# Optimization experiments

Measured on AMD Instinct MI355X. Metric: run time of the kernel, lower is better.

The kernel has to match this reference:

```python
import jax, jax.numpy as jnp
import numpy as np
from jax import lax

H = 100  # hidden size (hardcoded in the module)


def _lstm_cell(x, h, c, W_ih, W_hh, b):
    # gates: [B, 4H] in PyTorch order i, f, g, o
    gates = x @ W_ih.T + h @ W_hh.T + b
    i, f, g, o = jnp.split(gates, 4, axis=-1)
    c = jax.nn.sigmoid(f) * c + jax.nn.sigmoid(i) * jnp.tanh(g)
    h = jax.nn.sigmoid(o) * jnp.tanh(c)
    return h, c


def setup_inputs() -> dict:
    key = jax.random.key(0)
    ks = jax.random.split(key, 12)
    B, T = 512, 1000
    s = 0.1  # keep gates away from saturation
    return {
        "input": jax.random.normal(ks[0], (B, T), dtype=jnp.float32),
        "W_ih1": jax.random.normal(ks[1], (4 * H, 1), dtype=jnp.float32) * s,
        "W_hh1": jax.random.normal(ks[2], (4 * H, H), dtype=jnp.float32) * s,
        "b_ih1": jax.random.normal(ks[3], (4 * H,), dtype=jnp.float32) * s,
        "b_hh1": jax.random.normal(ks[4], (4 * H,), dtype=jnp.float32) * s,
        "W_ih2": jax.random.normal(ks[5], (4 * H, H), dtype=jnp.float32) * s,
        "W_hh2": jax.random.normal(ks[6], (4 * H, H), dtype=jnp.float32) * s,
        "b_ih2": jax.random.normal(ks[7], (4 * H,), dtype=jnp.float32) * s,
        "b_hh2": jax.random.normal(ks[8], (4 * H,), dtype=jnp.float32) * s,
        "W_lin": jax.random.normal(ks[9], (1, H), dtype=jnp.float32) * s,
        "b_lin": jax.random.normal(ks[10], (1,), dtype=jnp.float32) * s,
        "future": 300,
    }


def reference(input, W_ih1, W_hh1, b_ih1, b_hh1, W_ih2, W_hh2, b_ih2, b_hh2,
              W_lin, b_lin, future):
    B = input.shape[0]
    b1 = b_ih1 + b_hh1
    b2 = b_ih2 + b_hh2
    xs = input.T[:, :, None]  # [T, B, 1]
    z = jnp.zeros((B, H), dtype=input.dtype)

    def step(carry, x):
        h1, c1, h2, c2 = carry
        h1, c1 = _lstm_cell(x, h1, c1, W_ih1, W_hh1, b1)
        h2, c2 = _lstm_cell(h1, h2, c2, W_ih2, W_hh2, b2)
        y = h2 @ W_lin.T + b_lin  # [B, 1]
        return (h1, c1, h2, c2), y

    carry, ys = lax.scan(step, (z, z, z, z), xs)  # ys: [T, B, 1]

    def fstep(carry, _):
        h1, c1, h2, c2, y = carry
        h1, c1 = _lstm_cell(y, h1, c1, W_ih1, W_hh1, b1)
        h2, c2 = _lstm_cell(h1, h2, c2, W_ih2, W_hh2, b2)
        y = h2 @ W_lin.T + b_lin
        return (h1, c1, h2, c2, y), y

    h1, c1, h2, c2 = carry
    _, ys_f = lax.scan(fstep, (h1, c1, h2, c2, ys[-1]), None, length=future)

    out = jnp.concatenate([ys, ys_f], axis=0)  # [T+future, B, 1]
    return out[:, :, 0].T  # [B, T+future]
```

## Files before the change

kernel.cpp:

```cpp
#include <hip/hip_runtime.h>
#include <stdint.h>

#define HID 100
#define B_TOTAL 512
#define T_IN 1000
#define NB 2
#define BLOCK 512

typedef __fp16 f16x8 __attribute__((ext_vector_type(8)));
typedef float f32x4 __attribute__((ext_vector_type(4)));

#define MF(A, B, C) __builtin_amdgcn_mfma_f32_16x16x32_f16((A), (B), (C), 0, 0, 0)
#define Z4 ((f32x4){0.f, 0.f, 0.f, 0.f})

#if __has_builtin(__builtin_amdgcn_exp2f)
#define EXP2F(x) __builtin_amdgcn_exp2f(x)
#else
#define EXP2F(x) exp2f(x)
#endif
#if __has_builtin(__builtin_amdgcn_rcpf)
#define RCPF(x) __builtin_amdgcn_rcpf(x)
#else
#define RCPF(x) (1.0f / (x))
#endif
#define LOG2E 1.44269504f
__device__ __forceinline__ float sigm(float x) { return RCPF(1.0f + EXP2F(-LOG2E * x)); }
__device__ __forceinline__ float tanh_fast(float x) {
  return 1.0f - 2.0f * RCPF(EXP2F((2.0f * LOG2E) * x) + 1.0f);
}

__device__ __forceinline__ int jmap(int tl, int m) { return (m & 3) * 100 + 4 * tl + (m >> 2); }

__device__ __forceinline__ __fp16 w1e(const float* Whh1, const float* Wih1,
                                      const float* bih1, const float* bhh1, int j, int k) {
  if (k < 100) return (__fp16)Whh1[j * 100 + k];
  if (k == 100) return (__fp16)Wih1[j];
  if (k == 101 || k == 102) {
    float b = bih1[j] + bhh1[j];
    __fp16 hi = (__fp16)b;
    return (k == 101) ? hi : (__fp16)(b - (float)hi);
  }
  return (__fp16)0.0f;
}
__device__ __forceinline__ __fp16 w2e(const float* Wih2, const float* Whh2,
                                      const float* bih2, const float* bhh2, int j, int k) {
  if (k < 100) return (__fp16)Wih2[j * 100 + k];
  if (k == 101 || k == 102) {
    float b = bih2[j] + bhh2[j];
    __fp16 hi = (__fp16)b;
    return (k == 101) ? hi : (__fp16)(b - (float)hi);
  }
  if (k >= 112 && k < 212) return (__fp16)Whh2[j * 100 + (k - 112)];
  return (__fp16)0.0f;
}

__device__ __forceinline__ f16x8 mka1(const float* Whh1, const float* Wih1,
                                      const float* bih1, const float* bhh1,
                                      int tl, int kt, int m, int kg) {
  int j = jmap(tl, m);
  f16x8 r;
#pragma unroll
  for (int e = 0; e < 8; e++) r[e] = w1e(Whh1, Wih1, bih1, bhh1, j, kt * 32 + kg * 8 + e);
  return r;
}
__device__ __forceinline__ f16x8 mka2(const float* Wih2, const float* Whh2,
                                      const float* bih2, const float* bhh2,
                                      int tl, int kt, int m, int kg) {
  int j = jmap(tl, m);
  f16x8 r;
#pragma unroll
  for (int e = 0; e < 8; e++) r[e] = w2e(Wih2, Whh2, bih2, bhh2, j, kt * 32 + kg * 8 + e);
  return r;
}

__global__ __launch_bounds__(BLOCK, 2) void lstm2_mfma(
    const float* __restrict__ input,
    const float* __restrict__ Wih1,
    const float* __restrict__ Whh1,
    const float* __restrict__ bih1,
    const float* __restrict__ bhh1,
    const float* __restrict__ Wih2,
    const float* __restrict__ Whh2,
    const float* __restrict__ bih2,
    const float* __restrict__ bhh2,
    const float* __restrict__ Wlin,
    const float* __restrict__ blin,
    const int* __restrict__ futp,
    float* __restrict__ out)
{
  __shared__ __align__(16) __fp16 H1X[2][NB][128];
  __shared__ __align__(16) __fp16 H2s[2][NB][112];
  __shared__ __align__(16) float  ybuf[2][NB][104];
  __shared__ __align__(16) float  xrow[NB][T_IN];
  __shared__ __align__(16) __fp16 T24[11 * 64 * 8];
  __shared__ float wls[104];

  const int tid = threadIdx.x;
  const int lane = tid & 63;
  const int wv = tid >> 6;
  const int b0 = blockIdx.x * NB;
  const int F = futp[0];
  const int TT = T_IN + F;

  for (int i = tid; i < NB * T_IN; i += BLOCK) {
    int b = i / T_IN, tt = i % T_IN;
    xrow[b][tt] = input[(size_t)(b0 + b) * T_IN + tt];
  }
  { uint32_t* z = (uint32_t*)H1X; if (tid < 256) z[tid] = 0u; }
  { uint32_t* z = (uint32_t*)H2s; if (tid < 224) z[tid] = 0u; }
  { float* z = (float*)ybuf; if (tid < 416) z[tid] = 0.0f; }
  if (tid < 104) wls[tid] = (tid < HID) ? Wlin[tid] : 0.0f;

  const int n15 = lane & 15;
  const int kg = lane >> 4;
  const int bcol = lane & 1;

  const int sel = lane & 15;
  const int cg  = sel >> 1;
  const int ab  = sel & 1;
  const int aq  = lane >> 4;
  const int atl = (cg == 0) ? wv : (cg == 1) ? 8 + wv : (cg == 2) ? 16 + wv : 24;
  const int ak  = atl * 4 + aq;
  const bool awr1 = (sel < 6) || (wv == 0 && sel < 8);
  const bool awr2 = (sel < 6) || (wv == 1 && sel < 8);
  float c1v = 0.0f, c2v = 0.0f;

  const int is_y = (tid >= 496);
  const int ybat = ((tid - 496) >> 3) & 1;
  const int yl = (tid - 496) & 7;
  const float blin0 = blin[0];

  f16x8 W1f0[4], W1f1[4], W1f2[4], W2f0[7], W2f1[7], W2f2[7];
#pragma unroll
  for (int kt = 0; kt < 4; kt++) {
    W1f0[kt] = mka1(Whh1, Wih1, bih1, bhh1, wv, kt, n15, kg);
    W1f1[kt] = mka1(Whh1, Wih1, bih1, bhh1, 8 + wv, kt, n15, kg);
    W1f2[kt] = mka1(Whh1, Wih1, bih1, bhh1, 16 + wv, kt, n15, kg);
  }
#pragma unroll
  for (int kt = 0; kt < 7; kt++) {
    W2f0[kt] = mka2(Wih2, Whh2, bih2, bhh2, wv, kt, n15, kg);
    W2f1[kt] = mka2(Wih2, Whh2, bih2, bhh2, 8 + wv, kt, n15, kg);
    W2f2[kt] = mka2(Wih2, Whh2, bih2, bhh2, 16 + wv, kt, n15, kg);
  }
  if (tid < 64) {
    f16x8* TV = (f16x8*)T24;
    const int m_ = tid & 15, kg_ = tid >> 4;
#pragma unroll
    for (int kt = 0; kt < 4; kt++) TV[kt * 64 + tid] = mka1(Whh1, Wih1, bih1, bhh1, 24, kt, m_, kg_);
#pragma unroll
    for (int kt = 0; kt < 3; kt++) TV[(4 + kt) * 64 + tid] = mka2(Wih2, Whh2, bih2, bhh2, 24, 4 + kt, m_, kg_);
#pragma unroll
    for (int kt = 0; kt < 4; kt++) TV[(7 + kt) * 64 + tid] = mka2(Wih2, Whh2, bih2, bhh2, 24, kt, m_, kg_);
  }

  __syncthreads();
  if (tid < 4) { H1X[tid >> 1][tid & 1][101] = (__fp16)1.0f; H1X[tid >> 1][tid & 1][102] = (__fp16)1.0f; }
  if (tid >= 4 && tid < 6) H1X[1][tid - 4][100] = (__fp16)xrow[tid - 4][0];
  __syncthreads();

  f16x8 bL1[4], bH2[3], bL2[4];
  f32x4 c0, c1, c2, c3, d0, d1, d2, d3;

#define RD_L1(P) { _Pragma("unroll") for (int kt_ = 0; kt_ < 4; kt_++) \
    bL1[kt_] = *(const f16x8*)&H1X[P][bcol][kt_ * 32 + kg * 8]; }
#define RD_H2P(P) { _Pragma("unroll") for (int kt_ = 0; kt_ < 3; kt_++) \
    bH2[kt_] = *(const f16x8*)&H2s[P][bcol][16 + kt_ * 32 + kg * 8]; }
#define RD_L2(PH1, PH2) { _Pragma("unroll") for (int kt_ = 0; kt_ < 4; kt_++) { \
    const int k0_ = kt_ * 32 + kg * 8; \
    const __fp16* sp_ = (k0_ < 112) ? &H1X[PH1][bcol][k0_] : &H2s[PH2][bcol][k0_ - 112]; \
    bL2[kt_] = *(const f16x8*)sp_; } }

#define MFMA_L1 { \
    c0 = Z4; c1 = Z4; c2 = Z4; c3 = Z4; \
    _Pragma("unroll") for (int kt_ = 0; kt_ < 4; kt_++) { \
      c0 = MF(W1f0[kt_], bL1[kt_], c0); c1 = MF(W1f1[kt_], bL1[kt_], c1); c2 = MF(W1f2[kt_], bL1[kt_], c2); } \
    if (wv == 0) { const f16x8* TV = (const f16x8*)T24; \
      _Pragma("unroll") for (int kt_ = 0; kt_ < 4; kt_++) c3 = MF(TV[kt_ * 64 + lane], bL1[kt_], c3); } }

#define MFMA_L2 { \
    d0 = Z4; d1 = Z4; d2 = Z4; d3 = Z4; \
    _Pragma("unroll") for (int kt_ = 0; kt_ < 4; kt_++) { \
      d0 = MF(W2f0[kt_], bL2[kt_], d0); d1 = MF(W2f1[kt_], bL2[kt_], d1); d2 = MF(W2f2[kt_], bL2[kt_], d2); } \
    _Pragma("unroll") for (int kt_ = 0; kt_ < 3; kt_++) { \
      d0 = MF(W2f0[kt_ + 4], bH2[kt_], d0); d1 = MF(W2f1[kt_ + 4], bH2[kt_], d1); d2 = MF(W2f2[kt_ + 4], bH2[kt_], d2); } \
    if (wv == 1) { const f16x8* TV = (const f16x8*)T24; \
      _Pragma("unroll") for (int kt_ = 0; kt_ < 4; kt_++) d3 = MF(TV[(7 + kt_) * 64 + lane], bL2[kt_], d3); \
      _Pragma("unroll") for (int kt_ = 0; kt_ < 3; kt_++) d3 = MF(TV[(4 + kt_) * 64 + lane], bH2[kt_], d3); } }

#define ACT1(W_) { \
    f32x4 qq = (cg == 0) ? c0 : (cg == 1) ? c1 : (cg == 2) ? c2 : c3; \
    float sf_ = sigm(qq[1]), si_ = sigm(qq[0]), tg_ = tanh_fast(qq[2]); \
    c1v = sf_ * c1v + si_ * tg_; \
    float h_ = sigm(qq[3]) * tanh_fast(c1v); \
    if (awr1) H1X[W_][ab][ak] = (__fp16)h_; }

#define ACT2(W_) { \
    f32x4 qq = (cg == 0) ? d0 : (cg == 1) ? d1 : (cg == 2) ? d2 : d3; \
    float sf_ = sigm(qq[1]), si_ = sigm(qq[0]), tg_ = tanh_fast(qq[2]); \
    c2v = sf_ * c2v + si_ * tg_; \
    float h_ = sigm(qq[3]) * tanh_fast(c2v); \
    if (awr2) { H2s[W_][ab][ak] = (__fp16)h_; ybuf[W_][ab][ak] = h_; } }

#define Y_BODY(tt, RP, FEED, FP) { \
    const float* yb_ = &ybuf[RP][ybat][0]; \
    float s = 0.0f; \
    _Pragma("unroll") \
    for (int m = 0; m < 13; m++) s = fmaf(yb_[yl + 8 * m], wls[yl + 8 * m], s); \
    s += __shfl_down(s, 4, 8); \
    s += __shfl_down(s, 2, 8); \
    s += __shfl_down(s, 1, 8); \
    if (yl == 0) { \
      float y = s + blin0; \
      out[(size_t)(b0 + ybat) * TT + (tt)] = y; \
      if (FEED) H1X[FP][ybat][100] = (__fp16)y; } }

  RD_L1(1)
  MFMA_L1
  ACT1(0)
  if (tid >= 80 && tid < 82) H1X[0][tid - 80][100] = (__fp16)xrow[tid - 80][1];
  __syncthreads();

  for (int t = 0; t < T_IN - 1; t++) {
    const int p = t & 1, w = p ^ 1;
    RD_L1(p) RD_L2(p, p) RD_H2P(p)
    MFMA_L2
    MFMA_L1
    if (is_y && t > 0) Y_BODY(t - 1, p, 0, 0)
    if (tid >= 80 && tid < 82 && t + 2 < T_IN)
      H1X[w][tid - 80][100] = (__fp16)xrow[tid - 80][t + 2];
    ACT2(w)
    ACT1(w)
    __syncthreads();
  }

  for (int t = T_IN - 1; t < TT; t++) {
    const int P = t & 1, W = P ^ 1;
    RD_L2(P, P) RD_H2P(P)
    MFMA_L2
    if (is_y && t == T_IN - 1) Y_BODY(t - 1, P, 0, 0)
    ACT2(W)
    __syncthreads();
    if (is_y) Y_BODY(t, W, (t + 1) < TT, P)
    if (t + 1 >= TT) break;
    __syncthreads();
    RD_L1(P)
    MFMA_L1
    ACT1(W)
    __syncthreads();
  }
}

extern "C" void kernel_launch(void* const* d_in, const int* in_sizes, int n_in,
                              void* d_out, int out_size, void* d_ws, size_t ws_size,
                              hipStream_t stream) {
  const float* input = (const float*)d_in[0];
  const float* Wih1  = (const float*)d_in[1];
  const float* Whh1  = (const float*)d_in[2];
  const float* bih1  = (const float*)d_in[3];
  const float* bhh1  = (const float*)d_in[4];
  const float* Wih2  = (const float*)d_in[5];
  const float* Whh2  = (const float*)d_in[6];
  const float* bih2  = (const float*)d_in[7];
  const float* bhh2  = (const float*)d_in[8];
  const float* Wlin  = (const float*)d_in[9];
  const float* blin  = (const float*)d_in[10];
  const int*   futp  = (const int*)d_in[11];
  float* out = (float*)d_out;

  dim3 grid(B_TOTAL / NB);
  dim3 block(BLOCK);
  hipLaunchKernelGGL(lstm2_mfma, grid, block, 0, stream,
                     input, Wih1, Whh1, bih1, bhh1, Wih2, Whh2, bih2, bhh2,
                     Wlin, blin, futp, out);
}
```

Baseline: 1.660 ms.

## Restructure autoregressive phase to overlap layer-1 MFMA and compute output redundantly per wave

In the future-prediction loop, the layer-1 recurrent MFMA now runs alongside the layer-2 MFMA, with the x input column zeroed out of the weights. Each wave computes the linear output y itself with fdot2 over H2 from shared memory plus cross-lane shuffles, then adds y·W_ih1 as a rank-1 fma in the activation. This removes one barrier and the serial Y_BODY→L1 dependency per future step. Layer-2 operand reads also reuse the layer-1 h fragments instead of reloading them, and the shared buffers get a wider row stride.

```diff
diff --git a/kernel.cpp b/kernel.cpp
--- a/kernel.cpp
+++ b/kernel.cpp
@@ -6,8 +6,10 @@
 #define T_IN 1000
 #define NB 2
 #define BLOCK 512
+#define RSTR 160
 
 typedef __fp16 f16x8 __attribute__((ext_vector_type(8)));
+typedef __fp16 f16x2 __attribute__((ext_vector_type(2)));
 typedef float f32x4 __attribute__((ext_vector_type(4)));
 
 #define MF(A, B, C) __builtin_amdgcn_mfma_f32_16x16x32_f16((A), (B), (C), 0, 0, 0)
@@ -27,6 +29,21 @@
 __device__ __forceinline__ float sigm(float x) { return RCPF(1.0f + EXP2F(-LOG2E * x)); }
 __device__ __forceinline__ float tanh_fast(float x) {
   return 1.0f - 2.0f * RCPF(EXP2F((2.0f * LOG2E) * x) + 1.0f);
+}
+
+__device__ __forceinline__ float dot8(f16x8 a, f16x8 b, float acc) {
+#if __has_builtin(__builtin_amdgcn_fdot2)
+#pragma unroll
+  for (int q = 0; q < 4; q++) {
+    f16x2 xa = {a[2 * q], a[2 * q + 1]};
+    f16x2 xb = {b[2 * q], b[2 * q + 1]};
+    acc = __builtin_amdgcn_fdot2(xa, xb, acc, false);
+  }
+#else
+#pragma unroll
+  for (int e = 0; e < 8; e++) acc = fmaf((float)a[e], (float)b[e], acc);
+#endif
+  return acc;
 }
 
 __device__ __forceinline__ int jmap(int tl, int m) { return (m & 3) * 100 + 4 * tl + (m >> 2); }
@@ -88,8 +105,8 @@
     const int* __restrict__ futp,
     float* __restrict__ out)
 {
-  __shared__ __align__(16) __fp16 H1X[2][NB][128];
-  __shared__ __align__(16) __fp16 H2s[2][NB][112];
+  __shared__ __align__(16) __fp16 H1X[2][NB][RSTR];
+  __shared__ __align__(16) __fp16 H2s[2][NB][RSTR];
   __shared__ __align__(16) float  ybuf[2][NB][104];
   __shared__ __align__(16) float  xrow[NB][T_IN];
   __shared__ __align__(16) __fp16 T24[11 * 64 * 8];
@@ -106,8 +123,8 @@
     int b = i / T_IN, tt = i % T_IN;
     xrow[b][tt] = input[(size_t)(b0 + b) * T_IN + tt];
   }
-  { uint32_t* z = (uint32_t*)H1X; if (tid < 256) z[tid] = 0u; }
-  { uint32_t* z = (uint32_t*)H2s; if (tid < 224) z[tid] = 0u; }
+  { uint32_t* z = (uint32_t*)H1X; if (tid < 320) z[tid] = 0u; }
+  { uint32_t* z = (uint32_t*)H2s; if (tid < 320) z[tid] = 0u; }
   { float* z = (float*)ybuf; if (tid < 416) z[tid] = 0.0f; }
   if (tid < 104) wls[tid] = (tid < HID) ? Wlin[tid] : 0.0f;
 
@@ -130,6 +147,19 @@
   const int yl = (tid - 496) & 7;
   const float blin0 = blin[0];
 
+  f16x8 wlinv[4];
+#pragma unroll
+  for (int i = 0; i < 4; i++) {
+#pragma unroll
+    for (int e = 0; e < 8; e++) {
+      int k = i * 32 + kg * 8 + e;
+      wlinv[i][e] = (__fp16)((k < HID) ? Wlin[k] : 0.f);
+    }
+  }
+  f32x4 wih1q;
+#pragma unroll
+  for (int g = 0; g < 4; g++) wih1q[g] = Wih1[g * 100 + ak];
+
   f16x8 W1f0[4], W1f1[4], W1f2[4], W2f0[7], W2f1[7], W2f2[7];
 #pragma unroll
   for (int kt = 0; kt < 4; kt++) {
@@ -159,50 +189,59 @@
   if (tid >= 4 && tid < 6) H1X[1][tid - 4][100] = (__fp16)xrow[tid - 4][0];
   __syncthreads();
 
-  f16x8 bL1[4], bH2[3], bL2[4];
+  f16x8 bH1a[4], bH2[3], bl2m;
   f32x4 c0, c1, c2, c3, d0, d1, d2, d3;
 
-#define RD_L1(P) { _Pragma("unroll") for (int kt_ = 0; kt_ < 4; kt_++) \
-    bL1[kt_] = *(const f16x8*)&H1X[P][bcol][kt_ * 32 + kg * 8]; }
+#define RD_H1A(P) { _Pragma("unroll") for (int kt_ = 0; kt_ < 4; kt_++) \
+    bH1a[kt_] = *(const f16x8*)&H1X[P][bcol][kt_ * 32 + kg * 8]; }
+#define RD_L2M(P) { f16x8 hm_ = *(const f16x8*)&H2s[P][bcol][(kg >= 2) ? ((kg - 2) * 8) : 0]; \
+    bl2m = (kg >= 2) ? hm_ : bH1a[3]; }
 #define RD_H2P(P) { _Pragma("unroll") for (int kt_ = 0; kt_ < 3; kt_++) \
     bH2[kt_] = *(const f16x8*)&H2s[P][bcol][16 + kt_ * 32 + kg * 8]; }
-#define RD_L2(PH1, PH2) { _Pragma("unroll") for (int kt_ = 0; kt_ < 4; kt_++) { \
-    const int k0_ = kt_ * 32 + kg * 8; \
-    const __fp16* sp_ = (k0_ < 112) ? &H1X[PH1][bcol][k0_] : &H2s[PH2][bcol][k0_ - 112]; \
-    bL2[kt_] = *(const f16x8*)sp_; } }
 
 #define MFMA_L1 { \
     c0 = Z4; c1 = Z4; c2 = Z4; c3 = Z4; \
     _Pragma("unroll") for (int kt_ = 0; kt_ < 4; kt_++) { \
-      c0 = MF(W1f0[kt_], bL1[kt_], c0); c1 = MF(W1f1[kt_], bL1[kt_], c1); c2 = MF(W1f2[kt_], bL1[kt_], c2); } \
+      c0 = MF(W1f0[kt_], bH1a[kt_], c0); c1 = MF(W1f1[kt_], bH1a[kt_], c1); c2 = MF(W1f2[kt_], bH1a[kt_], c2); } \
     if (wv == 0) { const f16x8* TV = (const f16x8*)T24; \
-      _Pragma("unroll") for (int kt_ = 0; kt_ < 4; kt_++) c3 = MF(TV[kt_ * 64 + lane], bL1[kt_], c3); } }
+      _Pragma("unroll") for (int kt_ = 0; kt_ < 4; kt_++) c3 = MF(TV[kt_ * 64 + lane], bH1a[kt_], c3); } }
 
 #define MFMA_L2 { \
     d0 = Z4; d1 = Z4; d2 = Z4; d3 = Z4; \
-    _Pragma("unroll") for (int kt_ = 0; kt_ < 4; kt_++) { \
-      d0 = MF(W2f0[kt_], bL2[kt_], d0); d1 = MF(W2f1[kt_], bL2[kt_], d1); d2 = MF(W2f2[kt_], bL2[kt_], d2); } \
+    _Pragma("unroll") for (int kt_ = 0; kt_ < 3; kt_++) { \
+      d0 = MF(W2f0[kt_], bH1a[kt_], d0); d1 = MF(W2f1[kt_], bH1a[kt_], d1); d2 = MF(W2f2[kt_], bH1a[kt_], d2); } \
+    d0 = MF(W2f0[3], bl2m, d0); d1 = MF(W2f1[3], bl2m, d1); d2 = MF(W2f2[3], bl2m, d2); \
     _Pragma("unroll") for (int kt_ = 0; kt_ < 3; kt_++) { \
       d0 = MF(W2f0[kt_ + 4], bH2[kt_], d0); d1 = MF(W2f1[kt_ + 4], bH2[kt_], d1); d2 = MF(W2f2[kt_ + 4], bH2[kt_], d2); } \
     if (wv == 1) { const f16x8* TV = (const f16x8*)T24; \
-      _Pragma("unroll") for (int kt_ = 0; kt_ < 4; kt_++) d3 = MF(TV[(7 + kt_) * 64 + lane], bL2[kt_], d3); \
+      _Pragma("unroll") for (int kt_ = 0; kt_ < 3; kt_++) d3 = MF(TV[(7 + kt_) * 64 + lane], bH1a[kt_], d3); \
+      d3 = MF(TV[10 * 64 + lane], bl2m, d3); \
       _Pragma("unroll") for (int kt_ = 0; kt_ < 3; kt_++) d3 = MF(TV[(4 + kt_) * 64 + lane], bH2[kt_], d3); } }
 
-#define ACT1(W_) { \
+#define ACT1_TF(W_) { \
     f32x4 qq = (cg == 0) ? c0 : (cg == 1) ? c1 : (cg == 2) ? c2 : c3; \
     float sf_ = sigm(qq[1]), si_ = sigm(qq[0]), tg_ = tanh_fast(qq[2]); \
     c1v = sf_ * c1v + si_ * tg_; \
     float h_ = sigm(qq[3]) * tanh_fast(c1v); \
     if (awr1) H1X[W_][ab][ak] = (__fp16)h_; }
 
-#define ACT2(W_) { \
+#define ACT1_AR(W_, YV_) { \
+    f32x4 qq = (cg == 0) ? c0 : (cg == 1) ? c1 : (cg == 2) ? c2 : c3; \
+    qq[0] = fmaf(wih1q[0], (YV_), qq[0]); qq[1] = fmaf(wih1q[1], (YV_), qq[1]); \
+    qq[2] = fmaf(wih1q[2], (YV_), qq[2]); qq[3] = fmaf(wih1q[3], (YV_), qq[3]); \
+    float sf_ = sigm(qq[1]), si_ = sigm(qq[0]), tg_ = tanh_fast(qq[2]); \
+    c1v = sf_ * c1v + si_ * tg_; \
+    float h_ = sigm(qq[3]) * tanh_fast(c1v); \
+    if (awr1) H1X[W_][ab][ak] = (__fp16)h_; }
+
+#define ACT2(W_, YB_) { \
     f32x4 qq = (cg == 0) ? d0 : (cg == 1) ? d1 : (cg == 2) ? d2 : d3; \
     float sf_ = sigm(qq[1]), si_ = sigm(qq[0]), tg_ = tanh_fast(qq[2]); \
     c2v = sf_ * c2v + si_ * tg_; \
     float h_ = sigm(qq[3]) * tanh_fast(c2v); \
-    if (awr2) { H2s[W_][ab][ak] = (__fp16)h_; ybuf[W_][ab][ak] = h_; } }
-
-#define Y_BODY(tt, RP, FEED, FP) { \
+    if (awr2) { H2s[W_][ab][ak] = (__fp16)h_; if (YB_) ybuf[W_][ab][ak] = h_; } }
+
+#define Y_BODY(tt, RP) { \
     const float* yb_ = &ybuf[RP][ybat][0]; \
     float s = 0.0f; \
     _Pragma("unroll") \
@@ -210,43 +249,52 @@
     s += __shfl_down(s, 4, 8); \
     s += __shfl_down(s, 2, 8); \
     s += __shfl_down(s, 1, 8); \
-    if (yl == 0) { \
-      float y = s + blin0; \
-      out[(size_t)(b0 + ybat) * TT + (tt)] = y; \
-      if (FEED) H1X[FP][ybat][100] = (__fp16)y; } }
-
-  RD_L1(1)
+    if (yl == 0) out[(size_t)(b0 + ybat) * TT + (tt)] = s + blin0; }
+
+  RD_H1A(1)
   MFMA_L1
-  ACT1(0)
+  ACT1_TF(0)
   if (tid >= 80 && tid < 82) H1X[0][tid - 80][100] = (__fp16)xrow[tid - 80][1];
   __syncthreads();
 
   for (int t = 0; t < T_IN - 1; t++) {
     const int p = t & 1, w = p ^ 1;
-    RD_L1(p) RD_L2(p, p) RD_H2P(p)
+    RD_H1A(p) RD_L2M(p) RD_H2P(p)
     MFMA_L2
     MFMA_L1
-    if (is_y && t > 0) Y_BODY(t - 1, p, 0, 0)
+    if (is_y && t > 0) Y_BODY(t - 1, p)
     if (tid >= 80 && tid < 82 && t + 2 < T_IN)
       H1X[w][tid - 80][100] = (__fp16)xrow[tid - 80][t + 2];
-    ACT2(w)
-    ACT1(w)
+    ACT2(w, 1)
+    ACT1_TF(w)
     __syncthreads();
   }
 
+  if (kg == 0) {
+    W1f0[3][4] = (__fp16)0.f; W1f1[3][4] = (__fp16)0.f; W1f2[3][4] = (__fp16)0.f;
+  }
+  if (tid < 16) ((__fp16*)T24)[3 * 512 + tid * 8 + 4] = (__fp16)0.f;
+  __syncthreads();
+
   for (int t = T_IN - 1; t < TT; t++) {
-    const int P = t & 1, W = P ^ 1;
-    RD_L2(P, P) RD_H2P(P)
+    const int p = t & 1, w = p ^ 1;
+    RD_H1A(p) RD_L2M(p) RD_H2P(p)
     MFMA_L2
-    if (is_y && t == T_IN - 1) Y_BODY(t - 1, P, 0, 0)
-    ACT2(W)
+    MFMA_L1
+    if (is_y && t == T_IN - 1) Y_BODY(t - 1, p)
+    ACT2(w, 0)
     __syncthreads();
-    if (is_y) Y_BODY(t, W, (t + 1) < TT, P)
-    if (t + 1 >= TT) break;
-    __syncthreads();
-    RD_L1(P)
-    MFMA_L1
-    ACT1(W)
+    float s_ = 0.f;
+#pragma unroll
+    for (int i_ = 0; i_ < 4; i_++) {
+      f16x8 hh_ = *(const f16x8*)&H2s[w][bcol][i_ * 32 + kg * 8];
+      s_ = dot8(hh_, wlinv[i_], s_);
+    }
+    s_ += __shfl_xor(s_, 16, 64);
+    s_ += __shfl_xor(s_, 32, 64);
+    const float yv = s_ + blin0;
+    if (wv == 0 && lane < 2) out[(size_t)(b0 + lane) * TT + t] = yv;
+    ACT1_AR(w, yv)
     __syncthreads();
   }
 }
```

Result: faster. 1.576 ms (-5.0%).
